# Kernel tuning notes

Hardware: AMD Instinct MI355X
Metric: run time of the kernel (lower is better)

## Reference

```python
import jax, jax.numpy as jnp
import numpy as np

# Config mirroring init_kwargs
B, N, DM = 16, 512, 512          # batch, max_ast_len, hidden_size
PAR_HEADS, BRO_HEADS = 4, 4
H = PAR_HEADS + BRO_HEADS        # 8 heads
DK = DM // H                     # 64
R = 8                            # max_rel_pos
L = 2                            # num_layers
DFF = 4 * DM
EPS = 1e-5


def setup_inputs() -> dict:
    key = jax.random.key(0)
    ks = jax.random.split(key, 24)
    s = 0.02
    inp = {
        "src_emb": jax.random.normal(ks[0], (B, N, DM), jnp.float32),
        "par_edges": jax.random.randint(ks[1], (B, R, N), 0, N, jnp.int32),
        "bro_edges": jax.random.randint(ks[2], (B, R, N), 0, N, jnp.int32),
        # relative-position embedding tables (par heads ++ bro heads along head axis,
        # exactly what concat_vec(rel_par_*, rel_bro_*, dim=1) produces): [H, R, DK]
        "rel_q": s * jax.random.normal(ks[3], (H, R, DK), jnp.float32),
        "rel_k": s * jax.random.normal(ks[4], (H, R, DK), jnp.float32),
        "rel_v": s * jax.random.normal(ks[5], (H, R, DK), jnp.float32),
        # per-layer weights, stacked over layers
        "Wq": s * jax.random.normal(ks[6], (L, DM, DM), jnp.float32),
        "Wk": s * jax.random.normal(ks[7], (L, DM, DM), jnp.float32),
        "Wv": s * jax.random.normal(ks[8], (L, DM, DM), jnp.float32),
        "Wo": s * jax.random.normal(ks[9], (L, DM, DM), jnp.float32),
        "ln1_g": jnp.ones((L, DM), jnp.float32),
        "ln1_b": jnp.zeros((L, DM), jnp.float32),
        "W1": s * jax.random.normal(ks[10], (L, DM, DFF), jnp.float32),
        "b1": jnp.zeros((L, DFF), jnp.float32),
        "W2": s * jax.random.normal(ks[11], (L, DFF, DM), jnp.float32),
        "b2": jnp.zeros((L, DM), jnp.float32),
        "ln2_g": jnp.ones((L, DM), jnp.float32),
        "ln2_b": jnp.zeros((L, DM), jnp.float32),
        "normf_g": jnp.ones((DM,), jnp.float32),
        "normf_b": jnp.zeros((DM,), jnp.float32),
    }
    return inp


def _ln(x, g, b):
    m = x.mean(-1, keepdims=True)
    v = ((x - m) ** 2).mean(-1, keepdims=True)
    return (x - m) * jax.lax.rsqrt(v + EPS) * g + b


def _gather_nodes(t, idx):
    # t: [B,H,N,DK], idx: [B,H,R,N,1] -> [B,H,R,N,DK] gathered along node axis
    t_b = jnp.broadcast_to(t[:, :, None], (B, H, R, N, DK))
    return jnp.take_along_axis(t_b, idx, axis=3)


def _forward(src_emb, rel_q, rel_k, rel_v, Wq, Wk, Wv, Wo, ln1_g, ln1_b,
             W1, b1, W2, b2, ln2_g, ln2_b, normf_g, normf_b,
             par_edges, bro_edges):
    # start_nodes = concat_pos: repeat par edges over par heads, bro over bro heads
    start = jnp.concatenate(
        [jnp.repeat(par_edges[:, None], PAR_HEADS, axis=1),
         jnp.repeat(bro_edges[:, None], BRO_HEADS, axis=1)], axis=1)  # [B,H,R,N]
    idx = start[..., None].astype(jnp.int32)  # [B,H,R,N,1]
    scale = 1.0 / np.sqrt(DK)
    x = src_emb
    for i in range(L):
        q = (x @ Wq[i]).reshape(B, N, H, DK).transpose(0, 2, 1, 3)  # bhnd
        k = (x @ Wk[i]).reshape(B, N, H, DK).transpose(0, 2, 1, 3)
        v = (x @ Wv[i]).reshape(B, N, H, DK).transpose(0, 2, 1, 3)
        k_s = _gather_nodes(k, idx)  # [B,H,R,N,DK]
        v_s = _gather_nodes(v, idx)
        # Shaw-style relational scores over the R sparse neighbors only
        scores = (jnp.einsum('bhnd,bhrnd->bhrn', q, k_s)
                  + jnp.einsum('bhnd,hrd->bhrn', q, rel_k)
                  + jnp.einsum('hrd,bhrnd->bhrn', rel_q, k_s)) * scale
        attn = jax.nn.softmax(scores, axis=2)  # softmax over relative positions
        ctx = (jnp.einsum('bhrn,bhrnd->bhnd', attn, v_s)
               + jnp.einsum('bhrn,hrd->bhnd', attn, rel_v))
        ctx = ctx.transpose(0, 2, 1, 3).reshape(B, N, DM)
        x = _ln(x + ctx @ Wo[i], ln1_g[i], ln1_b[i])
        ff = jax.nn.relu(x @ W1[i] + b1[i]) @ W2[i] + b2[i]
        x = _ln(x + ff, ln2_g[i], ln2_b[i])
    return _ln(x, normf_g, normf_b)  # final self.norm


def reference(src_emb, par_edges, bro_edges, rel_q, rel_k, rel_v,
              Wq, Wk, Wv, Wo, ln1_g, ln1_b, W1, b1, W2, b2,
              ln2_g, ln2_b, normf_g, normf_b):
    return _forward(src_emb, rel_q, rel_k, rel_v, Wq, Wk, Wv, Wo,
                    ln1_g, ln1_b, W1, b1, W2, b2, ln2_g, ln2_b,
                    normf_g, normf_b, par_edges, bro_edges)
```

## Files before the change

### kernel.cpp

```cpp
#include <hip/hip_runtime.h>
#include <hip/hip_bf16.h>


#define BB 16
#define NN 512
#define DMM 512
#define HH 8
#define DKK 64
#define RR 8
#define LL 2
#define DFFV 2048
#define PAR_HEADS 4
#define EPSV 1e-5f

typedef __bf16 bf16x8 __attribute__((ext_vector_type(8)));
typedef float f32x4 __attribute__((ext_vector_type(4)));

__device__ __forceinline__ unsigned short f2bf(float f) {
    unsigned u = __float_as_uint(f);
    u += 0x7fff + ((u >> 16) & 1);
    return (unsigned short)(u >> 16);
}
__device__ __forceinline__ float bf2f(unsigned short u) {
    return __uint_as_float(((unsigned)u) << 16);
}

__global__ __launch_bounds__(256) void transpose_w_kernel(
    const float* __restrict__ src, unsigned short* __restrict__ dst,
    int K, int N, size_t zStride)
{
    __shared__ float tile[32][33];
    const float* s = src + (size_t)blockIdx.z * K * N;
    unsigned short* d = dst + (size_t)blockIdx.z * zStride;
    int k0 = blockIdx.y * 32, n0 = blockIdx.x * 32;
    int tx = threadIdx.x & 31, ty = threadIdx.x >> 5;
#pragma unroll
    for (int i = 0; i < 4; ++i)
        tile[ty + i * 8][tx] = s[(size_t)(k0 + ty + i * 8) * N + (n0 + tx)];
    __syncthreads();
#pragma unroll
    for (int i = 0; i < 4; ++i)
        d[(size_t)(n0 + ty + i * 8) * K + (k0 + tx)] = f2bf(tile[tx][ty + i * 8]);
}

__global__ __launch_bounds__(256) void convert_x_kernel(
    const float* __restrict__ src, float* __restrict__ x, unsigned short* __restrict__ xb, int n4)
{
    int i = blockIdx.x * blockDim.x + threadIdx.x;
    int stride = gridDim.x * blockDim.x;
    for (; i < n4; i += stride) {
        float4 f = ((const float4*)src)[i];
        ((float4*)x)[i] = f;
        ushort4 u;
        u.x = f2bf(f.x); u.y = f2bf(f.y); u.z = f2bf(f.z); u.w = f2bf(f.w);
        ((ushort4*)xb)[i] = u;
    }
}

template<int BM, int BN, int WM, int WN, bool OUTBF, bool DORELU>
__global__ __launch_bounds__(WM * WN * 64) void gemm_kernel(
    const unsigned short* __restrict__ A,
    const unsigned short* __restrict__ Bt,
    float* __restrict__ Cf,
    unsigned short* __restrict__ Cb,
    const float* __restrict__ bias,
    int M, int N, int K)
{
    constexpr int T = WM * WN * 64;
    constexpr int BK = 32;
    constexpr int TM = BM / WM, TN = BN / WN;
    __shared__ __align__(16) unsigned short As[BM * BK];
    __shared__ __align__(16) unsigned short Bs[BN * BK];
    int tid = threadIdx.x, lane = tid & 63, w = tid >> 6;
    int wr = w / WN, wc = w % WN;

    int gx = gridDim.x;
    int nwg = gx * gridDim.y;
    int flat = blockIdx.x + gx * blockIdx.y;
    int qq = nwg >> 3;
    int swz = (flat & 7) * qq + (flat >> 3);
    int bx = swz % gx, by = swz / gx;

    int mBase = by * BM, nBase = bx * BN;

    f32x4 acc[TM / 16][TN / 16];
#pragma unroll
    for (int i = 0; i < TM / 16; ++i)
#pragma unroll
        for (int j = 0; j < TN / 16; ++j) acc[i][j] = (f32x4){0.f, 0.f, 0.f, 0.f};

    for (int k0 = 0; k0 < K; k0 += BK) {
#pragma unroll
        for (int it = 0; it < BM * 4 / T; ++it) {
            int i = it * T + tid;
            int row = i >> 2, slot = i & 3;
            int gcol = (slot ^ ((row >> 1) & 3)) * 8;
            const unsigned short* ga = A + (size_t)(mBase + row) * K + k0 + gcol;
            __builtin_amdgcn_global_load_lds(
                (const __attribute__((address_space(1))) void*)ga,
                (__attribute__((address_space(3))) void*)(As + i * 8), 16, 0, 0);
        }
#pragma unroll
        for (int it = 0; it < BN * 4 / T; ++it) {
            int i = it * T + tid;
            int row = i >> 2, slot = i & 3;
            int gcol = (slot ^ ((row >> 1) & 3)) * 8;
            const unsigned short* gb = Bt + (size_t)(nBase + row) * K + k0 + gcol;
            __builtin_amdgcn_global_load_lds(
                (const __attribute__((address_space(1))) void*)gb,
                (__attribute__((address_space(3))) void*)(Bs + i * 8), 16, 0, 0);
        }
        __syncthreads();

        int s = lane >> 4, rsel = lane & 15;
        bf16x8 a[TM / 16], b[TN / 16];
#pragma unroll
        for (int m = 0; m < TM / 16; ++m) {
            int row = wr * TM + m * 16 + rsel;
            a[m] = *(const bf16x8*)((const char*)As + row * 64 + ((s ^ ((row >> 1) & 3)) << 4));
        }
#pragma unroll
        for (int n = 0; n < TN / 16; ++n) {
            int row = wc * TN + n * 16 + rsel;
            b[n] = *(const bf16x8*)((const char*)Bs + row * 64 + ((s ^ ((row >> 1) & 3)) << 4));
        }
#pragma unroll
        for (int m = 0; m < TM / 16; ++m)
#pragma unroll
            for (int n = 0; n < TN / 16; ++n)
                acc[m][n] = __builtin_amdgcn_mfma_f32_16x16x32_bf16(a[m], b[n], acc[m][n], 0, 0, 0);
        __syncthreads();
    }

    int rbase = (lane >> 4) * 4;
    int cloc = lane & 15;
#pragma unroll
    for (int m = 0; m < TM / 16; ++m) {
#pragma unroll
        for (int n = 0; n < TN / 16; ++n) {
            int col = nBase + wc * TN + n * 16 + cloc;
            float bv = bias ? bias[col] : 0.0f;
#pragma unroll
            for (int j = 0; j < 4; ++j) {
                int row = mBase + wr * TM + m * 16 + rbase + j;
                float val = acc[m][n][j] + bv;
                if (DORELU) val = fmaxf(val, 0.0f);
                if (OUTBF) Cb[(size_t)row * N + col] = f2bf(val);
                else       Cf[(size_t)row * N + col] = val;
            }
        }
    }
}

__global__ __launch_bounds__(256) void attn_kernel(
    const unsigned short* __restrict__ qkv,
    const int* __restrict__ par, const int* __restrict__ bro,
    const float* __restrict__ relq, const float* __restrict__ relk,
    const float* __restrict__ relv, unsigned short* __restrict__ cb)
{
    int wid = blockIdx.x * 4 + (threadIdx.x >> 6);
    int lane = threadIdx.x & 63;
    int n = wid & (NN - 1);
    int t = wid >> 9;
    int h = t & (HH - 1);
    int b = t >> 3;
    const int* edges = (h < PAR_HEADS) ? par : bro;

    float qd = bf2f(qkv[(size_t)(b * NN + n) * 1536 + h * DKK + lane]);
    float s[RR];
    int e[RR];
#pragma unroll
    for (int r = 0; r < RR; ++r) {
        e[r] = edges[(b * RR + r) * NN + n];
        float kd = bf2f(qkv[(size_t)(b * NN + e[r]) * 1536 + DMM + h * DKK + lane]);
        float rkd = relk[(h * RR + r) * DKK + lane];
        float rqd = relq[(h * RR + r) * DKK + lane];
        float tp = qd * kd + qd * rkd + rqd * kd;
#pragma unroll
        for (int off = 32; off > 0; off >>= 1) tp += __shfl_xor(tp, off, 64);
        s[r] = tp;
    }
    const float scale = 0.125f;
    float mx = -1e30f;
#pragma unroll
    for (int r = 0; r < RR; ++r) { s[r] *= scale; mx = fmaxf(mx, s[r]); }
    float denom = 0.f;
#pragma unroll
    for (int r = 0; r < RR; ++r) { s[r] = __expf(s[r] - mx); denom += s[r]; }
    float inv = 1.0f / denom;
    float od = 0.f;
#pragma unroll
    for (int r = 0; r < RR; ++r) {
        float vd = bf2f(qkv[(size_t)(b * NN + e[r]) * 1536 + 2 * DMM + h * DKK + lane]);
        float rvd = relv[(h * RR + r) * DKK + lane];
        od += s[r] * (vd + rvd);
    }
    od *= inv;
    cb[(size_t)(b * NN + n) * DMM + h * DKK + lane] = f2bf(od);
}

__global__ __launch_bounds__(256) void ln_kernel(
    const float* __restrict__ xin, const float* __restrict__ add,
    float* __restrict__ xout, unsigned short* __restrict__ xbout,
    const float* __restrict__ g, const float* __restrict__ bb)
{
    int row = blockIdx.x * 4 + (threadIdx.x >> 6);
    int lane = threadIdx.x & 63;
    const float* xr = xin + (size_t)row * DMM;
    const float* ar = add ? add + (size_t)row * DMM : nullptr;
    float vals[8];
    float s = 0.f;
#pragma unroll
    for (int j = 0; j < 8; ++j) {
        int c = lane + j * 64;
        float t = xr[c] + (ar ? ar[c] : 0.f);
        vals[j] = t;
        s += t;
    }
#pragma unroll
    for (int off = 32; off > 0; off >>= 1) s += __shfl_xor(s, off, 64);
    float mean = s * (1.0f / DMM);
    float s2 = 0.f;
#pragma unroll
    for (int j = 0; j < 8; ++j) { float d = vals[j] - mean; s2 += d * d; }
#pragma unroll
    for (int off = 32; off > 0; off >>= 1) s2 += __shfl_xor(s2, off, 64);
    float inv = rsqrtf(s2 * (1.0f / DMM) + EPSV);
#pragma unroll
    for (int j = 0; j < 8; ++j) {
        int c = lane + j * 64;
        float y = (vals[j] - mean) * inv * g[c] + bb[c];
        xout[(size_t)row * DMM + c] = y;
        if (xbout) xbout[(size_t)row * DMM + c] = f2bf(y);
    }
}

extern "C" void kernel_launch(void* const* d_in, const int* in_sizes, int n_in,
                              void* d_out, int out_size, void* d_ws, size_t ws_size,
                              hipStream_t stream)
{
    const float* src_emb = (const float*)d_in[0];
    const int*   par     = (const int*)d_in[1];
    const int*   bro     = (const int*)d_in[2];
    const float* rel_q   = (const float*)d_in[3];
    const float* rel_k   = (const float*)d_in[4];
    const float* rel_v   = (const float*)d_in[5];
    const float* Wq      = (const float*)d_in[6];
    const float* Wk      = (const float*)d_in[7];
    const float* Wv      = (const float*)d_in[8];
    const float* Wo      = (const float*)d_in[9];
    const float* ln1_g   = (const float*)d_in[10];
    const float* ln1_b   = (const float*)d_in[11];
    const float* W1      = (const float*)d_in[12];
    const float* b1      = (const float*)d_in[13];
    const float* W2      = (const float*)d_in[14];
    const float* b2      = (const float*)d_in[15];
    const float* ln2_g   = (const float*)d_in[16];
    const float* ln2_b   = (const float*)d_in[17];
    const float* normf_g = (const float*)d_in[18];
    const float* normf_b = (const float*)d_in[19];

    const size_t MB = 1024 * 1024;
    const int M = BB * NN;
    char* ws = (char*)d_ws;
    unsigned short* qkvb = (unsigned short*)(ws + 0 * MB);
    float*          t1   = (float*)(ws + 24 * MB);
    unsigned short* h1   = (unsigned short*)(ws + 40 * MB);
    unsigned short* xb   = (unsigned short*)(ws + 72 * MB);
    unsigned short* cbuf = (unsigned short*)(ws + 80 * MB);
    unsigned short* wqkvT = (unsigned short*)(ws + 88 * MB);
    unsigned short* woT  = wqkvT + (size_t)LL * 1536 * DMM;
    unsigned short* w1T  = woT + (size_t)LL * DMM * DMM;
    unsigned short* w2T  = w1T + (size_t)LL * DMM * DFFV;
    float* x = (float*)d_out;

    const size_t qkvStride = (size_t)1536 * DMM;
    transpose_w_kernel<<<dim3(DMM / 32, DMM / 32, LL), 256, 0, stream>>>(
        Wq, wqkvT + 0 * DMM * DMM, DMM, DMM, qkvStride);
    transpose_w_kernel<<<dim3(DMM / 32, DMM / 32, LL), 256, 0, stream>>>(
        Wk, wqkvT + 1 * DMM * DMM, DMM, DMM, qkvStride);
    transpose_w_kernel<<<dim3(DMM / 32, DMM / 32, LL), 256, 0, stream>>>(
        Wv, wqkvT + 2 * DMM * DMM, DMM, DMM, qkvStride);
    transpose_w_kernel<<<dim3(DMM / 32, DMM / 32, LL), 256, 0, stream>>>(
        Wo, woT, DMM, DMM, (size_t)DMM * DMM);
    transpose_w_kernel<<<dim3(DFFV / 32, DMM / 32, LL), 256, 0, stream>>>(
        W1, w1T, DMM, DFFV, (size_t)DMM * DFFV);
    transpose_w_kernel<<<dim3(DMM / 32, DFFV / 32, LL), 256, 0, stream>>>(
        W2, w2T, DFFV, DMM, (size_t)DMM * DFFV);

    convert_x_kernel<<<2048, 256, 0, stream>>>(src_emb, x, xb, M * DMM / 4);

    for (int l = 0; l < LL; ++l) {
        const unsigned short* wqkv_l = wqkvT + (size_t)l * 1536 * DMM;
        const unsigned short* wo_l = woT + (size_t)l * DMM * DMM;
        const unsigned short* w1_l = w1T + (size_t)l * DMM * DFFV;
        const unsigned short* w2_l = w2T + (size_t)l * DFFV * DMM;

        gemm_kernel<128, 128, 2, 2, true, false><<<dim3(1536 / 128, M / 128), 256, 0, stream>>>(
            xb, wqkv_l, nullptr, qkvb, nullptr, M, 1536, DMM);

        attn_kernel<<<BB * HH * NN / 4, 256, 0, stream>>>(qkvb, par, bro,
                                                          rel_q, rel_k, rel_v, cbuf);

        gemm_kernel<128, 64, 2, 2, false, false><<<dim3(512 / 64, M / 128), 256, 0, stream>>>(
            cbuf, wo_l, t1, nullptr, nullptr, M, DMM, DMM);
        ln_kernel<<<M / 4, 256, 0, stream>>>(x, t1, x, xb, ln1_g + l * DMM, ln1_b + l * DMM);

        gemm_kernel<128, 128, 2, 2, true, true><<<dim3(DFFV / 128, M / 128), 256, 0, stream>>>(
            xb, w1_l, nullptr, h1, b1 + l * DFFV, M, DFFV, DMM);
        gemm_kernel<128, 64, 2, 2, false, false><<<dim3(512 / 64, M / 128), 256, 0, stream>>>(
            h1, w2_l, t1, nullptr, b2 + l * DMM, M, DMM, DFFV);
        ln_kernel<<<M / 4, 256, 0, stream>>>(x, t1, x, xb, ln2_g + l * DMM, ln2_b + l * DMM);
    }

    ln_kernel<<<M / 4, 256, 0, stream>>>(x, nullptr, x, nullptr, normf_g, normf_b);
}
```

Baseline: 461.5 us.

## Use BK=64 GEMM tiles, split-K for N=512 GEMMs, and fuse weight transposes

The GEMM is rewritten with a fixed 128x64 tile and K-step 64, using 8-slot XOR swizzling so each barrier covers twice as many MFMAs. The two N=512 GEMMs (Wo and W2) now split K in two along grid z, writing fp32 partials that the LayerNorm kernel sums together with the bias. This roughly doubles the grid for the narrow GEMMs. The four QKVO weight transposes are merged into one launch. The cost is extra fp32 partial traffic, and the wider GEMMs (QKV, W1) now run with smaller 128x64 tiles, which lowers reuse.

```diff
diff --git a/kernel.cpp b/kernel.cpp
--- a/kernel.cpp
+++ b/kernel.cpp
@@ -25,6 +25,29 @@
     return __uint_as_float(((unsigned)u) << 16);
 }
 
+__global__ __launch_bounds__(256) void transpose_qkvo_kernel(
+    const float* __restrict__ Wq, const float* __restrict__ Wk,
+    const float* __restrict__ Wv, const float* __restrict__ Wo,
+    unsigned short* __restrict__ wqkvT, unsigned short* __restrict__ woT)
+{
+    __shared__ float tile[32][33];
+    int layer = blockIdx.z >> 2, which = blockIdx.z & 3;
+    const float* s = (which == 0 ? Wq : which == 1 ? Wk : which == 2 ? Wv : Wo)
+                     + (size_t)layer * DMM * DMM;
+    unsigned short* d = (which < 3)
+        ? wqkvT + (size_t)layer * 1536 * DMM + (size_t)which * DMM * DMM
+        : woT + (size_t)layer * DMM * DMM;
+    int k0 = blockIdx.y * 32, n0 = blockIdx.x * 32;
+    int tx = threadIdx.x & 31, ty = threadIdx.x >> 5;
+#pragma unroll
+    for (int i = 0; i < 4; ++i)
+        tile[ty + i * 8][tx] = s[(size_t)(k0 + ty + i * 8) * DMM + (n0 + tx)];
+    __syncthreads();
+#pragma unroll
+    for (int i = 0; i < 4; ++i)
+        d[(size_t)(n0 + ty + i * 8) * DMM + (k0 + tx)] = f2bf(tile[tx][ty + i * 8]);
+}
+
 __global__ __launch_bounds__(256) void transpose_w_kernel(
     const float* __restrict__ src, unsigned short* __restrict__ dst,
     int K, int N, size_t zStride)
@@ -57,22 +80,20 @@
     }
 }
 
-template<int BM, int BN, int WM, int WN, bool OUTBF, bool DORELU>
-__global__ __launch_bounds__(WM * WN * 64) void gemm_kernel(
+template<bool OUTBF, bool DORELU>
+__global__ __launch_bounds__(256) void gemm_kernel(
     const unsigned short* __restrict__ A,
     const unsigned short* __restrict__ Bt,
     float* __restrict__ Cf,
     unsigned short* __restrict__ Cb,
     const float* __restrict__ bias,
-    int M, int N, int K)
-{
-    constexpr int T = WM * WN * 64;
-    constexpr int BK = 32;
-    constexpr int TM = BM / WM, TN = BN / WN;
+    int M, int N, int K, int kLen)
+{
+    constexpr int BM = 128, BN = 64, BK = 64;
     __shared__ __align__(16) unsigned short As[BM * BK];
     __shared__ __align__(16) unsigned short Bs[BN * BK];
     int tid = threadIdx.x, lane = tid & 63, w = tid >> 6;
-    int wr = w / WN, wc = w % WN;
+    int wr = w >> 1, wc = w & 1;
 
     int gx = gridDim.x;
     int nwg = gx * gridDim.y;
@@ -80,31 +101,31 @@
     int qq = nwg >> 3;
     int swz = (flat & 7) * qq + (flat >> 3);
     int bx = swz % gx, by = swz / gx;
-
     int mBase = by * BM, nBase = bx * BN;
-
-    f32x4 acc[TM / 16][TN / 16];
-#pragma unroll
-    for (int i = 0; i < TM / 16; ++i)
-#pragma unroll
-        for (int j = 0; j < TN / 16; ++j) acc[i][j] = (f32x4){0.f, 0.f, 0.f, 0.f};
-
-    for (int k0 = 0; k0 < K; k0 += BK) {
-#pragma unroll
-        for (int it = 0; it < BM * 4 / T; ++it) {
-            int i = it * T + tid;
-            int row = i >> 2, slot = i & 3;
-            int gcol = (slot ^ ((row >> 1) & 3)) * 8;
+    int kStart = blockIdx.z * kLen;
+
+    f32x4 acc[4][2];
+#pragma unroll
+    for (int i = 0; i < 4; ++i)
+#pragma unroll
+        for (int j = 0; j < 2; ++j) acc[i][j] = (f32x4){0.f, 0.f, 0.f, 0.f};
+
+    for (int k0 = kStart; k0 < kStart + kLen; k0 += BK) {
+#pragma unroll
+        for (int it = 0; it < 4; ++it) {
+            int i = it * 256 + tid;
+            int row = i >> 3, slot = i & 7;
+            int gcol = (slot ^ (row & 7)) * 8;
             const unsigned short* ga = A + (size_t)(mBase + row) * K + k0 + gcol;
             __builtin_amdgcn_global_load_lds(
                 (const __attribute__((address_space(1))) void*)ga,
                 (__attribute__((address_space(3))) void*)(As + i * 8), 16, 0, 0);
         }
 #pragma unroll
-        for (int it = 0; it < BN * 4 / T; ++it) {
-            int i = it * T + tid;
-            int row = i >> 2, slot = i & 3;
-            int gcol = (slot ^ ((row >> 1) & 3)) * 8;
+        for (int it = 0; it < 2; ++it) {
+            int i = it * 256 + tid;
+            int row = i >> 3, slot = i & 7;
+            int gcol = (slot ^ (row & 7)) * 8;
             const unsigned short* gb = Bt + (size_t)(nBase + row) * K + k0 + gcol;
             __builtin_amdgcn_global_load_lds(
                 (const __attribute__((address_space(1))) void*)gb,
@@ -112,41 +133,52 @@
         }
         __syncthreads();
 
-        int s = lane >> 4, rsel = lane & 15;
-        bf16x8 a[TM / 16], b[TN / 16];
-#pragma unroll
-        for (int m = 0; m < TM / 16; ++m) {
-            int row = wr * TM + m * 16 + rsel;
-            a[m] = *(const bf16x8*)((const char*)As + row * 64 + ((s ^ ((row >> 1) & 3)) << 4));
-        }
-#pragma unroll
-        for (int n = 0; n < TN / 16; ++n) {
-            int row = wc * TN + n * 16 + rsel;
-            b[n] = *(const bf16x8*)((const char*)Bs + row * 64 + ((s ^ ((row >> 1) & 3)) << 4));
-        }
-#pragma unroll
-        for (int m = 0; m < TM / 16; ++m)
-#pragma unroll
-            for (int n = 0; n < TN / 16; ++n)
-                acc[m][n] = __builtin_amdgcn_mfma_f32_16x16x32_bf16(a[m], b[n], acc[m][n], 0, 0, 0);
+        int rsel = lane & 15, g0 = lane >> 4;
+        bf16x8 a[4][2], b[2][2];
+#pragma unroll
+        for (int m = 0; m < 4; ++m) {
+            int row = wr * 64 + m * 16 + rsel;
+#pragma unroll
+            for (int ks = 0; ks < 2; ++ks) {
+                int s = (g0 + ks * 4) ^ (row & 7);
+                a[m][ks] = *(const bf16x8*)((const char*)As + row * 128 + s * 16);
+            }
+        }
+#pragma unroll
+        for (int n = 0; n < 2; ++n) {
+            int row = wc * 32 + n * 16 + rsel;
+#pragma unroll
+            for (int ks = 0; ks < 2; ++ks) {
+                int s = (g0 + ks * 4) ^ (row & 7);
+                b[n][ks] = *(const bf16x8*)((const char*)Bs + row * 128 + s * 16);
+            }
+        }
+#pragma unroll
+        for (int m = 0; m < 4; ++m)
+#pragma unroll
+            for (int n = 0; n < 2; ++n)
+#pragma unroll
+                for (int ks = 0; ks < 2; ++ks)
+                    acc[m][n] = __builtin_amdgcn_mfma_f32_16x16x32_bf16(a[m][ks], b[n][ks], acc[m][n], 0, 0, 0);
         __syncthreads();
     }
 
+    size_t zoff = (size_t)blockIdx.z * M * N;
     int rbase = (lane >> 4) * 4;
     int cloc = lane & 15;
 #pragma unroll
-    for (int m = 0; m < TM / 16; ++m) {
-#pragma unroll
-        for (int n = 0; n < TN / 16; ++n) {
-            int col = nBase + wc * TN + n * 16 + cloc;
+    for (int m = 0; m < 4; ++m) {
+#pragma unroll
+        for (int n = 0; n < 2; ++n) {
+            int col = nBase + wc * 32 + n * 16 + cloc;
             float bv = bias ? bias[col] : 0.0f;
 #pragma unroll
             for (int j = 0; j < 4; ++j) {
-                int row = mBase + wr * TM + m * 16 + rbase + j;
+                int row = mBase + wr * 64 + m * 16 + rbase + j;
                 float val = acc[m][n][j] + bv;
                 if (DORELU) val = fmaxf(val, 0.0f);
-                if (OUTBF) Cb[(size_t)row * N + col] = f2bf(val);
-                else       Cf[(size_t)row * N + col] = val;
+                if (OUTBF) Cb[zoff + (size_t)row * N + col] = f2bf(val);
+                else       Cf[zoff + (size_t)row * N + col] = val;
             }
         }
     }
@@ -200,20 +232,25 @@
 }
 
 __global__ __launch_bounds__(256) void ln_kernel(
-    const float* __restrict__ xin, const float* __restrict__ add,
+    const float* __restrict__ xin, const float* __restrict__ add0,
+    const float* __restrict__ add1, const float* __restrict__ bias,
     float* __restrict__ xout, unsigned short* __restrict__ xbout,
     const float* __restrict__ g, const float* __restrict__ bb)
 {
     int row = blockIdx.x * 4 + (threadIdx.x >> 6);
     int lane = threadIdx.x & 63;
     const float* xr = xin + (size_t)row * DMM;
-    const float* ar = add ? add + (size_t)row * DMM : nullptr;
+    const float* a0 = add0 ? add0 + (size_t)row * DMM : nullptr;
+    const float* a1 = add1 ? add1 + (size_t)row * DMM : nullptr;
     float vals[8];
     float s = 0.f;
 #pragma unroll
     for (int j = 0; j < 8; ++j) {
         int c = lane + j * 64;
-        float t = xr[c] + (ar ? ar[c] : 0.f);
+        float t = xr[c];
+        if (a0) t += a0[c];
+        if (a1) t += a1[c];
+        if (bias) t += bias[c];
         vals[j] = t;
         s += t;
     }
@@ -263,26 +300,21 @@
     const size_t MB = 1024 * 1024;
     const int M = BB * NN;
     char* ws = (char*)d_ws;
+    float*          p    = (float*)(ws + 0 * MB);
     unsigned short* qkvb = (unsigned short*)(ws + 0 * MB);
-    float*          t1   = (float*)(ws + 24 * MB);
-    unsigned short* h1   = (unsigned short*)(ws + 40 * MB);
-    unsigned short* xb   = (unsigned short*)(ws + 72 * MB);
-    unsigned short* cbuf = (unsigned short*)(ws + 80 * MB);
-    unsigned short* wqkvT = (unsigned short*)(ws + 88 * MB);
+    unsigned short* h1   = (unsigned short*)(ws + 32 * MB);
+    unsigned short* xb   = (unsigned short*)(ws + 64 * MB);
+    unsigned short* cbuf = (unsigned short*)(ws + 72 * MB);
+    unsigned short* wqkvT = (unsigned short*)(ws + 80 * MB);
     unsigned short* woT  = wqkvT + (size_t)LL * 1536 * DMM;
     unsigned short* w1T  = woT + (size_t)LL * DMM * DMM;
     unsigned short* w2T  = w1T + (size_t)LL * DMM * DFFV;
+    float* p0 = p;
+    float* p1 = p + (size_t)M * DMM;
     float* x = (float*)d_out;
 
-    const size_t qkvStride = (size_t)1536 * DMM;
-    transpose_w_kernel<<<dim3(DMM / 32, DMM / 32, LL), 256, 0, stream>>>(
-        Wq, wqkvT + 0 * DMM * DMM, DMM, DMM, qkvStride);
-    transpose_w_kernel<<<dim3(DMM / 32, DMM / 32, LL), 256, 0, stream>>>(
-        Wk, wqkvT + 1 * DMM * DMM, DMM, DMM, qkvStride);
-    transpose_w_kernel<<<dim3(DMM / 32, DMM / 32, LL), 256, 0, stream>>>(
-        Wv, wqkvT + 2 * DMM * DMM, DMM, DMM, qkvStride);
-    transpose_w_kernel<<<dim3(DMM / 32, DMM / 32, LL), 256, 0, stream>>>(
-        Wo, woT, DMM, DMM, (size_t)DMM * DMM);
+    transpose_qkvo_kernel<<<dim3(16, 16, LL * 4), 256, 0, stream>>>(
+        Wq, Wk, Wv, Wo, wqkvT, woT);
     transpose_w_kernel<<<dim3(DFFV / 32, DMM / 32, LL), 256, 0, stream>>>(
         W1, w1T, DMM, DFFV, (size_t)DMM * DFFV);
     transpose_w_kernel<<<dim3(DMM / 32, DFFV / 32, LL), 256, 0, stream>>>(
@@ -296,22 +328,25 @@
         const unsigned short* w1_l = w1T + (size_t)l * DMM * DFFV;
         const unsigned short* w2_l = w2T + (size_t)l * DFFV * DMM;
 
-        gemm_kernel<128, 128, 2, 2, true, false><<<dim3(1536 / 128, M / 128), 256, 0, stream>>>(
-            xb, wqkv_l, nullptr, qkvb, nullptr, M, 1536, DMM);
+        gemm_kernel<true, false><<<dim3(1536 / 64, M / 128, 1), 256, 0, stream>>>(
+            xb, wqkv_l, nullptr, qkvb, nullptr, M, 1536, DMM, DMM);
 
         attn_kernel<<<BB * HH * NN / 4, 256, 0, stream>>>(qkvb, par, bro,
                                                           rel_q, rel_k, rel_v, cbuf);
 
-        gemm_kernel<128, 64, 2, 2, false, false><<<dim3(512 / 64, M / 128), 256, 0, stream>>>(
-            cbuf, wo_l, t1, nullptr, nullptr, M, DMM, DMM);
-        ln_kernel<<<M / 4, 256, 0, stream>>>(x, t1, x, xb, ln1_g + l * DMM, ln1_b + l * DMM);
-
-        gemm_kernel<128, 128, 2, 2, true, true><<<dim3(DFFV / 128, M / 128), 256, 0, stream>>>(
-            xb, w1_l, nullptr, h1, b1 + l * DFFV, M, DFFV, DMM);
-        gemm_kernel<128, 64, 2, 2, false, false><<<dim3(512 / 64, M / 128), 256, 0, stream>>>(
-            h1, w2_l, t1, nullptr, b2 + l * DMM, M, DMM, DFFV);
-        ln_kernel<<<M / 4, 256, 0, stream>>>(x, t1, x, xb, ln2_g + l * DMM, ln2_b + l * DMM);
-    }
-
-    ln_kernel<<<M / 4, 256, 0, stream>>>(x, nullptr, x, nullptr, normf_g, normf_b);
-}
+        gemm_kernel<false, false><<<dim3(512 / 64, M / 128, 2), 256, 0, stream>>>(
+            cbuf, wo_l, p, nullptr, nullptr, M, DMM, DMM, DMM / 2);
+        ln_kernel<<<M / 4, 256, 0, stream>>>(x, p0, p1, nullptr, x, xb,
+                                             ln1_g + l * DMM, ln1_b + l * DMM);
+
+        gemm_kernel<true, true><<<dim3(DFFV / 64, M / 128, 1), 256, 0, stream>>>(
+            xb, w1_l, nullptr, h1, b1 + l * DFFV, M, DFFV, DMM, DMM);
+        gemm_kernel<false, false><<<dim3(512 / 64, M / 128, 2), 256, 0, stream>>>(
+            h1, w2_l, p, nullptr, nullptr, M, DMM, DFFV, DFFV / 2);
+        ln_kernel<<<M / 4, 256, 0, stream>>>(x, p0, p1, b2 + l * DMM, x, xb,
+                                             ln2_g + l * DMM, ln2_b + l * DMM);
+    }
+
+    ln_kernel<<<M / 4, 256, 0, stream>>>(x, nullptr, nullptr, nullptr, x, nullptr,
+                                         normf_g, normf_b);
+}
```

Result: faster. 436.7 us (-5.4%).
